# Kernel optimization log

Measured on AMD Instinct MI355X. Metric: run time of the kernel, lower is better.

The kernel has to match this reference:

```python
import jax, jax.numpy as jnp
from jax import lax
import numpy as np
import math

B, N, M, SIG, HID, NFEAT, OUT, H = 256, 512, 16, 256, 256, 3, 10, 256
ALPHA, BETA = 1.0, 0.5


def setup_inputs() -> dict:
    key = jax.random.key(0)
    ks = jax.random.split(key, 12)
    s_g = 1.0 / math.sqrt(HID)
    s_f = 1.0 / math.sqrt(SIG)
    return {
        "x": jax.random.normal(ks[0], (B, 1, H, H), jnp.float32),
        "unif": jax.random.uniform(ks[1], (B, N), jnp.float32),
        "z": jax.random.normal(ks[2], (B, N, 2), jnp.float32),
        "m_g_params": jax.random.normal(ks[3], (1, 6 * M), jnp.float32),
        "gc1_w": jax.random.uniform(ks[4], (NFEAT, HID), jnp.float32, -s_g, s_g),
        "gc1_b": jax.random.uniform(ks[5], (HID,), jnp.float32, -s_g, s_g),
        "gc2_w": jax.random.uniform(ks[6], (HID, HID), jnp.float32, -s_g, s_g),
        "gc2_b": jax.random.uniform(ks[7], (HID,), jnp.float32, -s_g, s_g),
        "collapser1": 0.1 * jax.random.normal(ks[8], (SIG, N), jnp.float32),
        "collapser2": 0.1 * jax.random.normal(ks[9], (SIG, N), jnp.float32),
        "fcf_w": jax.random.uniform(ks[10], (OUT, SIG), jnp.float32, -s_f, s_f),
        "fcf_b": jax.random.uniform(ks[11], (OUT,), jnp.float32, -s_f, s_f),
    }


def _mixture_fields(m_g_params):
    # torch: split [num_sample, 6M] into M chunks of 6, stack -> [M, N, 6],
    # split along last dim, then .view(N, M) in C-order on the [M, N] field.
    raw = m_g_params.reshape(M, 6)  # [M, 6]
    return [jnp.broadcast_to(raw[:, j][:, None], (M, N)).reshape(N, M) for j in range(6)]


def reference(x, unif, z, m_g_params, gc1_w, gc1_b, gc2_w, gc2_b,
              collapser1, collapser2, fcf_w, fcf_b):
    pi_f, mux_f, muy_f, sx_f, sy_f, rho_f = _mixture_fields(m_g_params)
    pi = jax.nn.softmax(pi_f, axis=-1)            # [N, M]
    # categorical sampling via CDF inversion, vectorized over batch
    cdf = jnp.cumsum(pi, axis=-1)                 # [N, M]
    idx = jnp.argmax(unif[:, :, None] < cdf[None], axis=-1)  # [B, N]
    row = jnp.arange(N)[None, :]
    gat = lambda f: f[row, idx]                   # [B, N]
    mux, muy = gat(mux_f), gat(muy_f)
    sx, sy = jnp.exp(gat(sx_f)), jnp.exp(gat(sy_f))
    rho = jnp.tanh(gat(rho_f))
    # reparameterized bivariate-normal sample via Cholesky (lower)
    z1, z2 = z[..., 0], z[..., 1]
    xs = mux + sx * z1
    ys = muy + sy * (rho * z1 + jnp.sqrt(1.0 - rho * rho) * z2)
    # torch MVN.sample() is no_grad -> detach samples
    xs_c, ys_c = lax.stop_gradient(xs), lax.stop_gradient(ys)
    dx, dy = xs_c - mux, ys_c - muy
    omr2 = 1.0 - rho * rho
    quad = (dx * dx / (sx * sx) - 2.0 * rho * dx * dy / (sx * sy) + dy * dy / (sy * sy)) / omr2
    logprob = (-jnp.log(2.0 * jnp.pi) - jnp.log(sx * sy)
               - 0.5 * jnp.log(omr2) - 0.5 * quad)  # [B, N]
    full_log_prob = logprob.sum(axis=-1)           # [B]
    loc = jnp.tanh(jnp.stack([xs_c, ys_c], axis=-1))  # [B, N, 2]
    # adjacency: inverse shifted pairwise squared distance
    diff = loc[:, :, None, :] - loc[:, None, :, :]  # [B, N, N, 2]
    adj = 1.0 / (ALPHA + BETA * jnp.sum(diff * diff, axis=-1))  # [B, N, N]
    # pixel gather: denormalize (trunc toward zero, like torch .long())
    pix = jnp.trunc(0.5 * (loc + 1.0) * H - 0.1).astype(jnp.int32)
    pix = jnp.clip(pix, 0, H - 1)
    bidx = jnp.arange(B)[:, None]
    pv = x[bidx, :, pix[..., 0], pix[..., 1]]      # [B, N, 1]
    feat = jnp.concatenate([pv, loc], axis=-1)     # [B, N, 3]
    # GCN (eval mode: no dropout)
    s1 = jax.nn.relu(jnp.einsum('bnm,bmh->bnh', adj, feat @ gc1_w) + gc1_b)
    s2 = jax.nn.relu(jnp.einsum('bnm,bmh->bnh', adj, s1 @ gc2_w) + gc2_b)
    # nn.Softmax() (no dim) on 3D input resolves to dim=0 in torch
    g1 = jax.nn.softmax(jnp.einsum('sn,bnh->bsh', collapser1, s1), axis=0)
    g2 = jax.nn.softmax(jnp.einsum('sn,bnh->bsh', collapser2, s2), axis=0)
    sig = (g1 + g2).sum(axis=2)                    # [B, SIG]
    out = jax.nn.softmax(sig @ fcf_w.T + fcf_b, axis=-1)  # [B, OUT]
    return out, full_log_prob
```

## Files before the change

kernel.cpp:

```cpp
#include <hip/hip_runtime.h>
#include <hip/hip_bf16.h>
#include <math.h>

#define Bx   256
#define Nx   512
#define SIGx 256
#define HIDx 256
#define OUTx 10
#define Hx   256

typedef __attribute__((ext_vector_type(4))) float f32x4;
typedef long fp8x8;
typedef unsigned char uchar;

__device__ inline uchar f2fp8(float v) {
    int r = __builtin_amdgcn_cvt_pk_fp8_f32(v, 0.0f, 0, false);
    return (uchar)(r & 0xff);
}
__device__ inline uint pk4fp8(float a0, float a1, float a2, float a3) {
    int r = __builtin_amdgcn_cvt_pk_fp8_f32(a0, a1, 0, false);
    r = __builtin_amdgcn_cvt_pk_fp8_f32(a2, a3, r, true);
    return (uint)r;
}

__device__ inline void gload_lds16(const uchar* g, uchar* l) {
    __builtin_amdgcn_global_load_lds(
        (const __attribute__((address_space(1))) uint*)g,
        (__attribute__((address_space(3))) uint*)l, 16, 0, 0);
}
__device__ inline const uchar* laddr(const uchar* base, int row, int kb) {
    int ps = (kb >> 4) ^ ((row >> 1) & 3) ^ ((row >> 4) & 3);
    return base + row*64 + ps*16 + (kb & 15);
}

__global__ __launch_bounds__(512) void kA_sample(
    const float* __restrict__ x, const float* __restrict__ z,
    const float* __restrict__ mg, float* __restrict__ feat,
    float* __restrict__ flp)
{
    int b = blockIdx.x;
    int n = threadIdx.x;
    int g = n >> 5;
    float mux = mg[g*6+1];
    float muy = mg[g*6+2];
    float sxv = expf(mg[g*6+3]);
    float syv = expf(mg[g*6+4]);
    float rho = tanhf(mg[g*6+5]);
    float z1 = z[((size_t)b*Nx + n)*2 + 0];
    float z2 = z[((size_t)b*Nx + n)*2 + 1];
    float omr2 = 1.0f - rho*rho;
    float xs = mux + sxv*z1;
    float ys = muy + syv*(rho*z1 + sqrtf(omr2)*z2);
    float dx = xs - mux, dy = ys - muy;
    float quad = (dx*dx/(sxv*sxv) - 2.0f*rho*dx*dy/(sxv*syv) + dy*dy/(syv*syv)) / omr2;
    float logprob = -1.8378770664093453f - logf(sxv*syv) - 0.5f*logf(omr2) - 0.5f*quad;
    float lx = tanhf(xs), ly = tanhf(ys);
    int px = (int)truncf(0.5f*(lx+1.0f)*(float)Hx - 0.1f);
    int py = (int)truncf(0.5f*(ly+1.0f)*(float)Hx - 0.1f);
    px = px < 0 ? 0 : (px > Hx-1 ? Hx-1 : px);
    py = py < 0 ? 0 : (py > Hx-1 ? Hx-1 : py);
    float pv = x[(size_t)b*Hx*Hx + (size_t)px*Hx + py];
    size_t fo = ((size_t)b*Nx + n)*3;
    feat[fo+0] = pv; feat[fo+1] = lx; feat[fo+2] = ly;

    __shared__ float red[512];
    red[n] = logprob;
    __syncthreads();
    for (int st = 256; st > 0; st >>= 1) {
        if (n < st) red[n] += red[n+st];
        __syncthreads();
    }
    if (n == 0) flp[b] = red[0];
}

__global__ __launch_bounds__(256) void kPrep(
    const float* __restrict__ c1, const float* __restrict__ c2,
    const float* __restrict__ w2,
    uchar* __restrict__ c1q, uchar* __restrict__ c2q, uchar* __restrict__ w2tq)
{
    int idx = blockIdx.x*256 + threadIdx.x;
    if (idx < SIGx*Nx) {
        c1q[idx] = f2fp8(16.0f * c1[idx]);
        c2q[idx] = f2fp8(16.0f * c2[idx]);
    }
    if (idx < HIDx*HIDx) {
        int i = idx >> 8, j = idx & 255;
        w2tq[idx] = f2fp8(16.0f * w2[j*HIDx + i]);
    }
}

__global__ __launch_bounds__(512) void kFuse1(
    const float* __restrict__ featL, const float* __restrict__ w1,
    const float* __restrict__ b1,
    uchar* __restrict__ adjAll, uchar* __restrict__ s1tAll)
{
    int b = blockIdx.x;
    const float* fb = featL + (size_t)b*Nx*3;
    uchar* adj = adjAll + (size_t)b*Nx*Nx;
    uchar* s1t = s1tAll + (size_t)b*HIDx*Nx;

    __shared__ float fpv[Nx], flx[Nx], fly[Nx], fH[Nx];
    __shared__ float w1s[3*HIDx], b1s[HIDx];
    __shared__ float Gp[4][3][Nx];

    int t = threadIdx.x;
    {
        float pv = fb[t*3+0], lx = fb[t*3+1], ly = fb[t*3+2];
        fpv[t] = pv; flx[t] = lx; fly[t] = ly;
        fH[t] = fmaf(0.5f*lx, lx, fmaf(0.5f*ly, ly, 1.0f));
    }
    for (int i = t; i < 3*HIDx; i += 512) w1s[i] = w1[i];
    if (t < HIDx) b1s[t] = b1[t];
    __syncthreads();

    int tq = t & 127;
    int mc = t >> 7;
    int n4 = tq*4;

    float xn[4], yn[4], cn[4];
    #pragma unroll
    for (int e = 0; e < 4; ++e) {
        xn[e] = flx[n4+e]; yn[e] = fly[n4+e];
        cn[e] = fmaf(0.5f*xn[e], xn[e], 0.5f*yn[e]*yn[e]);
    }
    float G0[4] = {}, G1[4] = {}, G2[4] = {};

    int m0 = mc*128;
    #pragma unroll 4
    for (int mm = 0; mm < 128; ++mm) {
        int m = m0 + mm;
        float hx = fH[m], fx = flx[m], fy = fly[m];
        float a[4];
        #pragma unroll
        for (int e = 0; e < 4; ++e) {
            float s = fmaf(-yn[e], fy, fmaf(-xn[e], fx, hx + cn[e]));
            a[e] = __builtin_amdgcn_rcpf(s);
            G0[e] = fmaf(a[e], fpv[m], G0[e]);
            G1[e] = fmaf(a[e], fx, G1[e]);
            G2[e] = fmaf(a[e], fy, G2[e]);
        }
        *(uint*)(adj + (size_t)m*Nx + n4) = pk4fp8(a[0], a[1], a[2], a[3]);
    }

    *(f32x4*)&Gp[mc][0][n4] = (f32x4){G0[0],G0[1],G0[2],G0[3]};
    *(f32x4*)&Gp[mc][1][n4] = (f32x4){G1[0],G1[1],G1[2],G1[3]};
    *(f32x4*)&Gp[mc][2][n4] = (f32x4){G2[0],G2[1],G2[2],G2[3]};
    __syncthreads();

    f32x4 T0 = {}, T1 = {}, T2 = {};
    #pragma unroll
    for (int j = 0; j < 4; ++j) {
        T0 += *(const f32x4*)&Gp[j][0][n4];
        T1 += *(const f32x4*)&Gp[j][1][n4];
        T2 += *(const f32x4*)&Gp[j][2][n4];
    }

    int hc = mc;
    #pragma unroll 4
    for (int hh = 0; hh < 64; ++hh) {
        int h = hc*64 + hh;
        float w0 = w1s[h], wA = w1s[HIDx+h], wB = w1s[2*HIDx+h], bb = b1s[h];
        float v0 = fminf(fmaxf(fmaf(T0.x,w0, fmaf(T1.x,wA, fmaf(T2.x,wB, bb))), 0.0f), 448.0f);
        float v1 = fminf(fmaxf(fmaf(T0.y,w0, fmaf(T1.y,wA, fmaf(T2.y,wB, bb))), 0.0f), 448.0f);
        float v2 = fminf(fmaxf(fmaf(T0.z,w0, fmaf(T1.z,wA, fmaf(T2.z,wB, bb))), 0.0f), 448.0f);
        float v3 = fminf(fmaxf(fmaf(T0.w,w0, fmaf(T1.w,wA, fmaf(T2.w,wB, bb))), 0.0f), 448.0f);
        *(uint*)(s1t + (size_t)h*Nx + n4) = pk4fp8(v0, v1, v2, v3);
    }
}

__global__ __launch_bounds__(256) void kGemmAdjQ(
    const uchar* __restrict__ Aall, const uchar* __restrict__ adjAll,
    const float* __restrict__ bias, uchar* __restrict__ outAll)
{
    int b    = blockIdx.x;
    int tile = blockIdx.y;
    int rt = tile >> 2;
    int ct = tile & 3;
    const uchar* A = Aall + (size_t)b*HIDx*Nx;
    const uchar* Badj = adjAll + (size_t)b*Nx*Nx;
    uchar* outp = outAll + (size_t)b*HIDx*Nx;

    __shared__ __align__(16) uchar Als[128*64];
    __shared__ __align__(16) uchar Bls[128*64];
    int t = threadIdx.x;
    int lane = t & 63, wave = t >> 6;
    int wr = wave >> 1, wc = wave & 1;
    int q = lane >> 4, c16 = lane & 15;
    int r0 = rt*128, n0 = ct*128;
    int lrow = lane >> 2;
    int pu   = lane & 3;
    f32x4 acc[4][4] = {};

    for (int kk = 0; kk < Nx; kk += 64) {
        #pragma unroll
        for (int r = 0; r < 2; ++r) {
            int chunk = wave*2 + r;
            int row = chunk*16 + lrow;
            int sl = pu ^ ((row>>1)&3) ^ ((row>>4)&3);
            gload_lds16(A + (size_t)(r0+row)*Nx + kk + sl*16, Als + chunk*1024);
            gload_lds16(Badj + (size_t)(n0+row)*Nx + kk + sl*16, Bls + chunk*1024);
        }
        __syncthreads();
        #pragma unroll
        for (int ks = 0; ks < 64; ks += 32) {
            fp8x8 af[4], bfr[4];
            #pragma unroll
            for (int i = 0; i < 4; ++i)
                af[i] = *(const fp8x8*)laddr(Als, wr*64 + i*16 + c16, ks + q*8);
            #pragma unroll
            for (int j = 0; j < 4; ++j)
                bfr[j] = *(const fp8x8*)laddr(Bls, wc*64 + j*16 + c16, ks + q*8);
            #pragma unroll
            for (int i = 0; i < 4; ++i)
                #pragma unroll
                for (int j = 0; j < 4; ++j)
                    acc[i][j] = __builtin_amdgcn_mfma_f32_16x16x32_fp8_fp8(af[i], bfr[j], acc[i][j], 0, 0, 0);
        }
        __syncthreads();
    }
    #pragma unroll
    for (int i = 0; i < 4; ++i) {
        int rowb = r0 + wr*64 + i*16 + q*4;
        #pragma unroll
        for (int j = 0; j < 4; ++j) {
            int col = n0 + wc*64 + j*16 + c16;
            #pragma unroll
            for (int r = 0; r < 4; ++r) {
                float v = fmaxf(acc[i][j][r] + bias[rowb + r], 0.0f) * 0.25f;
                outp[(size_t)(rowb + r)*Nx + col] = f2fp8(fminf(v, 448.0f));
            }
        }
    }
}

template<int K, int NC, bool TRB>
__global__ __launch_bounds__(256) void kGstdQ(
    const uchar* __restrict__ Ash, const uchar* __restrict__ Ball,
    uchar* __restrict__ outAll, float oscale)
{
    constexpr int CT = NC / 128;
    int b    = blockIdx.x;
    int tile = blockIdx.y;
    int rt = tile / CT;
    int ct = tile % CT;
    const uchar* B = Ball + (size_t)b*HIDx*Nx;
    uchar* outp = outAll + (size_t)b*HIDx*NC;

    __shared__ __align__(16) uchar Als[128*64];
    __shared__ __align__(16) uchar Bls[128*64];
    int t = threadIdx.x;
    int lane = t & 63, wave = t >> 6;
    int wr = wave >> 1, wc = wave & 1;
    int q = lane >> 4, c16 = lane & 15;
    int r0 = rt*128, n0 = ct*128;
    int lrow = lane >> 2;
    int pu   = lane & 3;
    f32x4 acc[4][4] = {};

    for (int kk = 0; kk < K; kk += 64) {
        #pragma unroll
        for (int r = 0; r < 2; ++r) {
            int chunk = wave*2 + r;
            int row = chunk*16 + lrow;
            int sl = pu ^ ((row>>1)&3) ^ ((row>>4)&3);
            gload_lds16(Ash + (size_t)(r0+row)*K + kk + sl*16, Als + chunk*1024);
            if (!TRB)
                gload_lds16(B + (size_t)(n0+row)*K + kk + sl*16, Bls + chunk*1024);
        }
        if (TRB) {
            int pi  = t & 31;
            int nc8 = t >> 5;
            int hk = kk + 2*pi;
            const uchar* g0 = B + (size_t)hk*NC + n0 + nc8*16;
            const uchar* g1 = g0 + NC;
            float4 v0 = *(const float4*)g0;
            float4 v1 = *(const float4*)g1;
            const uchar* pa = (const uchar*)&v0;
            const uchar* qa = (const uchar*)&v1;
            int kb = 2*pi;
            int s  = kb >> 4;
            #pragma unroll
            for (int e = 0; e < 16; ++e) {
                int row = nc8*16 + e;
                int ps = s ^ ((row>>1)&3) ^ ((row>>4)&3);
                *(ushort*)(Bls + row*64 + ps*16 + (kb & 15)) =
                    (ushort)pa[e] | ((ushort)qa[e] << 8);
            }
        }
        __syncthreads();
        #pragma unroll
        for (int ks = 0; ks < 64; ks += 32) {
            fp8x8 af[4], bfr[4];
            #pragma unroll
            for (int i = 0; i < 4; ++i)
                af[i] = *(const fp8x8*)laddr(Als, wr*64 + i*16 + c16, ks + q*8);
            #pragma unroll
            for (int j = 0; j < 4; ++j)
                bfr[j] = *(const fp8x8*)laddr(Bls, wc*64 + j*16 + c16, ks + q*8);
            #pragma unroll
            for (int i = 0; i < 4; ++i)
                #pragma unroll
                for (int j = 0; j < 4; ++j)
                    acc[i][j] = __builtin_amdgcn_mfma_f32_16x16x32_fp8_fp8(af[i], bfr[j], acc[i][j], 0, 0, 0);
        }
        __syncthreads();
    }
    #pragma unroll
    for (int i = 0; i < 4; ++i) {
        int rowb = r0 + wr*64 + i*16 + q*4;
        #pragma unroll
        for (int j = 0; j < 4; ++j) {
            int col = n0 + wc*64 + j*16 + c16;
            #pragma unroll
            for (int r = 0; r < 4; ++r) {
                float v = acc[i][j][r] * oscale;
                v = fminf(fmaxf(v, -448.0f), 448.0f);
                outp[(size_t)(rowb + r)*NC + col] = f2fp8(v);
            }
        }
    }
}

__global__ __launch_bounds__(512) void kF1q(
    const uchar* __restrict__ t1, const uchar* __restrict__ t2,
    float* __restrict__ m1, float* __restrict__ rd1,
    float* __restrict__ m2, float* __restrict__ rd2)
{
    int s = blockIdx.x;
    int t = threadIdx.x;
    int hq = t & 63;
    int bq = t >> 6;
    const size_t str = (size_t)SIGx*HIDx;
    size_t base = (size_t)(bq*32)*str + (size_t)s*HIDx + hq*4;

    float mv1[4], dv1[4], mv2[4], dv2[4];
    #pragma unroll
    for (int e = 0; e < 4; ++e) { mv1[e]=-3.0e38f; dv1[e]=0.0f; mv2[e]=-3.0e38f; dv2[e]=0.0f; }

    for (int i = 0; i < 32; ++i) {
        uint u1 = *(const uint*)(t1 + base + (size_t)i*str);
        uint u2 = *(const uint*)(t2 + base + (size_t)i*str);
        float v1[4], v2[4];
        v1[0] = __builtin_amdgcn_cvt_f32_fp8(u1, 0);
        v1[1] = __builtin_amdgcn_cvt_f32_fp8(u1, 1);
        v1[2] = __builtin_amdgcn_cvt_f32_fp8(u1, 2);
        v1[3] = __builtin_amdgcn_cvt_f32_fp8(u1, 3);
        v2[0] = __builtin_amdgcn_cvt_f32_fp8(u2, 0);
        v2[1] = __builtin_amdgcn_cvt_f32_fp8(u2, 1);
        v2[2] = __builtin_amdgcn_cvt_f32_fp8(u2, 2);
        v2[3] = __builtin_amdgcn_cvt_f32_fp8(u2, 3);
        #pragma unroll
        for (int e = 0; e < 4; ++e) {
            float mn;
            mn = fmaxf(mv1[e], v1[e]);
            dv1[e] = dv1[e]*__expf(mv1[e]-mn) + __expf(v1[e]-mn); mv1[e] = mn;
            mn = fmaxf(mv2[e], v2[e]);
            dv2[e] = dv2[e]*__expf(mv2[e]-mn) + __expf(v2[e]-mn); mv2[e] = mn;
        }
    }

    __shared__ float pm1[8][256], pd1[8][256], pm2[8][256], pd2[8][256];
    #pragma unroll
    for (int e = 0; e < 4; ++e) {
        pm1[bq][hq*4+e] = mv1[e]; pd1[bq][hq*4+e] = dv1[e];
        pm2[bq][hq*4+e] = mv2[e]; pd2[bq][hq*4+e] = dv2[e];
    }
    __syncthreads();

    if (t < 256) {
        int h = t;
        float m = -3.0e38f, d = 0.0f;
        #pragma unroll
        for (int j = 0; j < 8; ++j) {
            float mm = pm1[j][h], dd = pd1[j][h];
            float mn = fmaxf(m, mm);
            d = d*__expf(m-mn) + dd*__expf(mm-mn);
            m = mn;
        }
        size_t o = (size_t)s*HIDx + h;
        m1[o] = m; rd1[o] = 1.0f/d;
    } else {
        int h = t - 256;
        float m = -3.0e38f, d = 0.0f;
        #pragma unroll
        for (int j = 0; j < 8; ++j) {
            float mm = pm2[j][h], dd = pd2[j][h];
            float mn = fmaxf(m, mm);
            d = d*__expf(m-mn) + dd*__expf(mm-mn);
            m = mn;
        }
        size_t o = (size_t)s*HIDx + h;
        m2[o] = m; rd2[o] = 1.0f/d;
    }
}

__global__ __launch_bounds__(256) void kF2q(
    const uchar* __restrict__ t1, const uchar* __restrict__ t2,
    const float* __restrict__ m1, const float* __restrict__ rd1,
    const float* __restrict__ m2, const float* __restrict__ rd2,
    float* __restrict__ sig)
{
    int b = blockIdx.y;
    int sq = threadIdx.x >> 6;
    int s = blockIdx.x*4 + sq;
    int hq = threadIdx.x & 63;
    size_t sh = (size_t)s*HIDx + hq*4;
    size_t tb = ((size_t)b*SIGx + s)*HIDx + hq*4;
    uint u1 = *(const uint*)(t1 + tb);
    uint u2 = *(const uint*)(t2 + tb);
    f32x4 a1 = *(const f32x4*)&m1[sh];
    f32x4 r1 = *(const f32x4*)&rd1[sh];
    f32x4 a2 = *(const f32x4*)&m2[sh];
    f32x4 r2 = *(const f32x4*)&rd2[sh];
    float v = 0.0f;
    v += __expf(__builtin_amdgcn_cvt_f32_fp8(u1,0) - a1.x) * r1.x;
    v += __expf(__builtin_amdgcn_cvt_f32_fp8(u1,1) - a1.y) * r1.y;
    v += __expf(__builtin_amdgcn_cvt_f32_fp8(u1,2) - a1.z) * r1.z;
    v += __expf(__builtin_amdgcn_cvt_f32_fp8(u1,3) - a1.w) * r1.w;
    v += __expf(__builtin_amdgcn_cvt_f32_fp8(u2,0) - a2.x) * r2.x;
    v += __expf(__builtin_amdgcn_cvt_f32_fp8(u2,1) - a2.y) * r2.y;
    v += __expf(__builtin_amdgcn_cvt_f32_fp8(u2,2) - a2.z) * r2.z;
    v += __expf(__builtin_amdgcn_cvt_f32_fp8(u2,3) - a2.w) * r2.w;

    __shared__ float red[256];
    red[threadIdx.x] = v;
    __syncthreads();
    for (int st = 32; st > 0; st >>= 1) {
        if (hq < st) red[threadIdx.x] += red[threadIdx.x + st];
        __syncthreads();
    }
    if (hq == 0) sig[(size_t)b*SIGx + s] = red[sq*64];
}

__global__ __launch_bounds__(256) void kG_out(
    const float* __restrict__ sig, const float* __restrict__ fw,
    const float* __restrict__ fb, float* __restrict__ out)
{
    int b = blockIdx.x;
    int tid = threadIdx.x;
    __shared__ float red[256];
    __shared__ float logits[OUTx];
    float sv = sig[(size_t)b*SIGx + tid];
    for (int o = 0; o < OUTx; ++o) {
        red[tid] = sv * fw[o*SIGx + tid];
        __syncthreads();
        for (int st = 128; st > 0; st >>= 1) {
            if (tid < st) red[tid] += red[tid+st];
            __syncthreads();
        }
        if (tid == 0) logits[o] = red[0] + fb[o];
        __syncthreads();
    }
    if (tid == 0) {
        float mx = logits[0];
        for (int o = 1; o < OUTx; ++o) mx = fmaxf(mx, logits[o]);
        float dd = 0.0f; float e[OUTx];
        for (int o = 0; o < OUTx; ++o) { e[o] = expf(logits[o]-mx); dd += e[o]; }
        float inv = 1.0f/dd;
        for (int o = 0; o < OUTx; ++o) out[(size_t)b*OUTx + o] = e[o]*inv;
    }
}

static inline size_t alignup(size_t b) { return (b + 255) & ~(size_t)255; }

extern "C" void kernel_launch(void* const* d_in, const int* in_sizes, int n_in,
                              void* d_out, int out_size, void* d_ws, size_t ws_size,
                              hipStream_t stream)
{
    const float* x   = (const float*)d_in[0];
    const float* z   = (const float*)d_in[2];
    const float* mg  = (const float*)d_in[3];
    const float* w1  = (const float*)d_in[4];
    const float* b1  = (const float*)d_in[5];
    const float* w2  = (const float*)d_in[6];
    const float* b2  = (const float*)d_in[7];
    const float* c1  = (const float*)d_in[8];
    const float* c2  = (const float*)d_in[9];
    const float* fw  = (const float*)d_in[10];
    const float* fbv = (const float*)d_in[11];
    float* out = (float*)d_out;
    float* flp = out + (size_t)Bx*OUTx;
    (void)in_sizes; (void)n_in; (void)out_size;

    char* ws = (char*)d_ws;
    size_t off = 0;
    auto alloc = [&](size_t bytes) -> char* {
        char* p = ws + off; off += alignup(bytes); return p;
    };
    float*  feat = (float*)alloc((size_t)Bx*Nx*3*4);
    uchar*  c1q  = (uchar*)alloc((size_t)SIGx*Nx);
    uchar*  c2q  = (uchar*)alloc((size_t)SIGx*Nx);
    uchar*  w2tq = (uchar*)alloc((size_t)HIDx*HIDx);
    uchar*  t1   = (uchar*)alloc((size_t)Bx*SIGx*HIDx);
    uchar*  t2   = (uchar*)alloc((size_t)Bx*SIGx*HIDx);
    float*  m1   = (float*)alloc((size_t)SIGx*HIDx*4);
    float*  d1   = (float*)alloc((size_t)SIGx*HIDx*4);
    float*  m2   = (float*)alloc((size_t)SIGx*HIDx*4);
    float*  d2   = (float*)alloc((size_t)SIGx*HIDx*4);
    float*  sig  = (float*)alloc((size_t)Bx*SIGx*4);
    size_t fixed = off;

    int BC = 1;
    for (int c = Bx; c >= 1; c >>= 1) {
        size_t need = fixed + alignup((size_t)c*Nx*Nx)
                            + 2*alignup((size_t)c*HIDx*Nx);
        if (need <= ws_size) { BC = c; break; }
    }
    uchar* Padj = (uchar*)alloc((size_t)BC*Nx*Nx);
    uchar* P1   = (uchar*)alloc((size_t)BC*HIDx*Nx);
    uchar* P2   = (uchar*)alloc((size_t)BC*HIDx*Nx);

    hipLaunchKernelGGL(kA_sample, dim3(Bx), dim3(Nx), 0, stream, x, z, mg, feat, flp);
    hipLaunchKernelGGL(kPrep, dim3(512), dim3(256), 0, stream, c1, c2, w2, c1q, c2q, w2tq);

    const int nch = Bx / BC;
    for (int c = 0; c < nch; ++c) {
        int b0 = c * BC;
        const float* featL = feat + (size_t)b0*Nx*3;
        uchar* t1L = t1 + (size_t)b0*SIGx*HIDx;
        uchar* t2L = t2 + (size_t)b0*SIGx*HIDx;
        hipLaunchKernelGGL(kFuse1, dim3(BC), dim3(512), 0, stream,
                           featL, w1, b1, Padj, P2);
        hipLaunchKernelGGL((kGstdQ<512,256,false>), dim3(BC, 4), dim3(256), 0, stream,
                           c1q, P2, t1L, 0.0625f);
        hipLaunchKernelGGL((kGstdQ<256,512,true>), dim3(BC, 8), dim3(256), 0, stream,
                           w2tq, P2, P1, 0.0625f);
        hipLaunchKernelGGL(kGemmAdjQ, dim3(BC, 8), dim3(256), 0, stream, P1, Padj, b2, P2);
        hipLaunchKernelGGL((kGstdQ<512,256,false>), dim3(BC, 4), dim3(256), 0, stream,
                           c2q, P2, t2L, 0.25f);
    }

    hipLaunchKernelGGL(kF1q, dim3(SIGx), dim3(512), 0, stream,
                       t1, t2, m1, d1, m2, d2);
    hipLaunchKernelGGL(kF2q, dim3(SIGx/4, Bx), dim3(256), 0, stream,
                       t1, t2, m1, d1, m2, d2, sig);
    hipLaunchKernelGGL(kG_out, dim3(Bx), dim3(256), 0, stream, sig, fw, fbv, out);
}
```

Measured before the change: 291.6 us.

## Recompute adjacency tiles in GEMM instead of materializing fp8 adjacency matrix

The layer-2 adjacency GEMM no longer reads a precomputed fp8 B×N×N adjacency buffer from global memory. kFuse1 now writes only per-node location data (x, y, half-norm terms), and kGemmAdjR regenerates each 128×64 adjacency tile in LDS with reciprocals before the MFMA loop. This removes about 64 MB of global writes and reads per pass, at the cost of extra ALU and rcp work in the GEMM and a padded 72-byte LDS row stride for the B tile. The workspace sizing also drops the adjacency buffer, which may allow larger batch chunks.

```diff
diff --git a/kernel.cpp b/kernel.cpp
--- a/kernel.cpp
+++ b/kernel.cpp
@@ -92,11 +92,11 @@
 __global__ __launch_bounds__(512) void kFuse1(
     const float* __restrict__ featL, const float* __restrict__ w1,
     const float* __restrict__ b1,
-    uchar* __restrict__ adjAll, uchar* __restrict__ s1tAll)
+    f32x4* __restrict__ locpL, uchar* __restrict__ s1tAll)
 {
     int b = blockIdx.x;
     const float* fb = featL + (size_t)b*Nx*3;
-    uchar* adj = adjAll + (size_t)b*Nx*Nx;
+    f32x4* locb = locpL + (size_t)b*Nx;
     uchar* s1t = s1tAll + (size_t)b*HIDx*Nx;
 
     __shared__ float fpv[Nx], flx[Nx], fly[Nx], fH[Nx];
@@ -107,7 +107,9 @@
     {
         float pv = fb[t*3+0], lx = fb[t*3+1], ly = fb[t*3+2];
         fpv[t] = pv; flx[t] = lx; fly[t] = ly;
-        fH[t] = fmaf(0.5f*lx, lx, fmaf(0.5f*ly, ly, 1.0f));
+        float hx = fmaf(0.5f*lx, lx, fmaf(0.5f*ly, ly, 1.0f));
+        fH[t] = hx;
+        locb[t] = (f32x4){lx, ly, hx, fmaf(0.5f*lx, lx, 0.5f*ly*ly)};
     }
     for (int i = t; i < 3*HIDx; i += 512) w1s[i] = w1[i];
     if (t < HIDx) b1s[t] = b1[t];
@@ -139,7 +141,6 @@
             G1[e] = fmaf(a[e], fx, G1[e]);
             G2[e] = fmaf(a[e], fy, G2[e]);
         }
-        *(uint*)(adj + (size_t)m*Nx + n4) = pk4fp8(a[0], a[1], a[2], a[3]);
     }
 
     *(f32x4*)&Gp[mc][0][n4] = (f32x4){G0[0],G0[1],G0[2],G0[3]};
@@ -168,8 +169,8 @@
     }
 }
 
-__global__ __launch_bounds__(256) void kGemmAdjQ(
-    const uchar* __restrict__ Aall, const uchar* __restrict__ adjAll,
+__global__ __launch_bounds__(256) void kGemmAdjR(
+    const uchar* __restrict__ Aall, const f32x4* __restrict__ locp,
     const float* __restrict__ bias, uchar* __restrict__ outAll)
 {
     int b    = blockIdx.x;
@@ -177,11 +178,11 @@
     int rt = tile >> 2;
     int ct = tile & 3;
     const uchar* A = Aall + (size_t)b*HIDx*Nx;
-    const uchar* Badj = adjAll + (size_t)b*Nx*Nx;
+    const f32x4* locB = locp + (size_t)b*Nx;
     uchar* outp = outAll + (size_t)b*HIDx*Nx;
 
     __shared__ __align__(16) uchar Als[128*64];
-    __shared__ __align__(16) uchar Bls[128*64];
+    __shared__ __align__(16) uchar Bls[128*72];
     int t = threadIdx.x;
     int lane = t & 63, wave = t >> 6;
     int wr = wave >> 1, wc = wave & 1;
@@ -189,16 +190,34 @@
     int r0 = rt*128, n0 = ct*128;
     int lrow = lane >> 2;
     int pu   = lane & 3;
+
+    int row = t & 127;
+    int kb0 = __builtin_amdgcn_readfirstlane((t >> 7) * 32);
+    f32x4 nd = locB[n0 + row];
+    float xn = nd.x, yn = nd.y, cnv = nd.w;
+    uchar* brow = Bls + row*72;
+
     f32x4 acc[4][4] = {};
 
     for (int kk = 0; kk < Nx; kk += 64) {
         #pragma unroll
         for (int r = 0; r < 2; ++r) {
             int chunk = wave*2 + r;
-            int row = chunk*16 + lrow;
-            int sl = pu ^ ((row>>1)&3) ^ ((row>>4)&3);
-            gload_lds16(A + (size_t)(r0+row)*Nx + kk + sl*16, Als + chunk*1024);
-            gload_lds16(Badj + (size_t)(n0+row)*Nx + kk + sl*16, Bls + chunk*1024);
+            int srow = chunk*16 + lrow;
+            int sl = pu ^ ((srow>>1)&3) ^ ((srow>>4)&3);
+            gload_lds16(A + (size_t)(r0+srow)*Nx + kk + sl*16, Als + chunk*1024);
+        }
+        const f32x4* mp = locB + kk + kb0;
+        #pragma unroll
+        for (int i = 0; i < 8; ++i) {
+            f32x4 m0 = mp[i*4+0], m1 = mp[i*4+1], m2 = mp[i*4+2], m3 = mp[i*4+3];
+            float s0 = fmaf(-yn, m0.y, fmaf(-xn, m0.x, m0.z + cnv));
+            float s1 = fmaf(-yn, m1.y, fmaf(-xn, m1.x, m1.z + cnv));
+            float s2 = fmaf(-yn, m2.y, fmaf(-xn, m2.x, m2.z + cnv));
+            float s3 = fmaf(-yn, m3.y, fmaf(-xn, m3.x, m3.z + cnv));
+            *(uint*)(brow + kb0 + i*4) = pk4fp8(
+                __builtin_amdgcn_rcpf(s0), __builtin_amdgcn_rcpf(s1),
+                __builtin_amdgcn_rcpf(s2), __builtin_amdgcn_rcpf(s3));
         }
         __syncthreads();
         #pragma unroll
@@ -209,7 +228,7 @@
                 af[i] = *(const fp8x8*)laddr(Als, wr*64 + i*16 + c16, ks + q*8);
             #pragma unroll
             for (int j = 0; j < 4; ++j)
-                bfr[j] = *(const fp8x8*)laddr(Bls, wc*64 + j*16 + c16, ks + q*8);
+                bfr[j] = *(const fp8x8*)(Bls + (size_t)(wc*64 + j*16 + c16)*72 + ks + q*8);
             #pragma unroll
             for (int i = 0; i < 4; ++i)
                 #pragma unroll
@@ -488,6 +507,7 @@
         char* p = ws + off; off += alignup(bytes); return p;
     };
     float*  feat = (float*)alloc((size_t)Bx*Nx*3*4);
+    f32x4*  locp = (f32x4*)alloc((size_t)Bx*Nx*16);
     uchar*  c1q  = (uchar*)alloc((size_t)SIGx*Nx);
     uchar*  c2q  = (uchar*)alloc((size_t)SIGx*Nx);
     uchar*  w2tq = (uchar*)alloc((size_t)HIDx*HIDx);
@@ -502,11 +522,9 @@
 
     int BC = 1;
     for (int c = Bx; c >= 1; c >>= 1) {
-        size_t need = fixed + alignup((size_t)c*Nx*Nx)
-                            + 2*alignup((size_t)c*HIDx*Nx);
+        size_t need = fixed + 2*alignup((size_t)c*HIDx*Nx);
         if (need <= ws_size) { BC = c; break; }
     }
-    uchar* Padj = (uchar*)alloc((size_t)BC*Nx*Nx);
     uchar* P1   = (uchar*)alloc((size_t)BC*HIDx*Nx);
     uchar* P2   = (uchar*)alloc((size_t)BC*HIDx*Nx);
 
@@ -517,15 +535,17 @@
     for (int c = 0; c < nch; ++c) {
         int b0 = c * BC;
         const float* featL = feat + (size_t)b0*Nx*3;
+        f32x4* locpL = locp + (size_t)b0*Nx;
         uchar* t1L = t1 + (size_t)b0*SIGx*HIDx;
         uchar* t2L = t2 + (size_t)b0*SIGx*HIDx;
         hipLaunchKernelGGL(kFuse1, dim3(BC), dim3(512), 0, stream,
-                           featL, w1, b1, Padj, P2);
+                           featL, w1, b1, locpL, P2);
         hipLaunchKernelGGL((kGstdQ<512,256,false>), dim3(BC, 4), dim3(256), 0, stream,
                            c1q, P2, t1L, 0.0625f);
         hipLaunchKernelGGL((kGstdQ<256,512,true>), dim3(BC, 8), dim3(256), 0, stream,
                            w2tq, P2, P1, 0.0625f);
-        hipLaunchKernelGGL(kGemmAdjQ, dim3(BC, 8), dim3(256), 0, stream, P1, Padj, b2, P2);
+        hipLaunchKernelGGL(kGemmAdjR, dim3(BC, 8), dim3(256), 0, stream,
+                           P1, locpL, b2, P2);
         hipLaunchKernelGGL((kGstdQ<512,256,false>), dim3(BC, 4), dim3(256), 0, stream,
                            c2q, P2, t2L, 0.25f);
     }
```

Result: slower. 302.9 us (+3.9%).
